# Kernel tuning notes

Hardware: AMD Instinct MI355X
Metric: run time of the kernel (lower is better)

Reference implementation:

```python
import jax, jax.numpy as jnp
import numpy as np

ALPHA = 0.2  # LeakyReLU negative slope
N, F_IN, F_OUT = 8192, 512, 64
NEG_INF = -9e15


def setup_inputs() -> dict:
    key = jax.random.key(0)
    k1, k2, k3, k4 = jax.random.split(key, 4)
    inp = jax.random.normal(k1, (N, F_IN), dtype=jnp.float32)
    adj = jax.random.randint(k2, (N, N), 0, 2, dtype=jnp.int32)
    W = jax.random.normal(k3, (F_IN, F_OUT), dtype=jnp.float32) * (1.414 / np.sqrt(F_IN))
    a = jax.random.normal(k4, (2 * F_OUT, 1), dtype=jnp.float32) * 0.1
    return {"input": inp, "adj": adj, "W": W, "a": a, "sparse": 0}


def reference(input, adj, W, a, sparse):
    h = input @ W  # [N, F_out]
    # Decompose concat([h_i, h_j]) @ a into additive src/dst terms (same math,
    # avoids the O(N^2 * 2F) intermediate): e_ij = leakyrelu(h_i@a1 + h_j@a2)
    f_src = h @ a[:F_OUT]   # [N, 1]
    f_dst = h @ a[F_OUT:]   # [N, 1]
    e = jax.nn.leaky_relu(f_src + f_dst.T, ALPHA)  # [N, N]
    attention = jnp.where(adj > 0, e, NEG_INF)
    attention = jax.nn.softmax(attention, axis=1)
    h_prime = attention @ h  # [N, F_out]
    return jax.nn.leaky_relu(h_prime, 0.01)[None]  # concat=True path; default F.leaky_relu slope 0.01
```

## Files before the change

### kernel.cpp

```cpp
#include <hip/hip_runtime.h>
#include <hip/hip_bf16.h>

#define N 8192
#define FIN 512
#define FOUT 64
#define ALPHA 0.2f

typedef __bf16 bf16x8 __attribute__((ext_vector_type(8)));
typedef float f32x4 __attribute__((ext_vector_type(4)));
typedef int i32x4 __attribute__((ext_vector_type(4)));


__device__ __forceinline__ unsigned enc_f(float x) {
    unsigned u = __float_as_uint(x);
    return (u & 0x80000000u) ? ~u : (u | 0x80000000u);
}
__device__ __forceinline__ float dec_f(unsigned u) {
    return (u & 0x80000000u) ? __uint_as_float(u & 0x7FFFFFFFu) : __uint_as_float(~u);
}

__global__ __launch_bounds__(64) void k_wt(const float* __restrict__ W,
                                           __bf16* __restrict__ WtG) {
    const int g = blockIdx.x * 64 + threadIdx.x;
    const int k = g >> 3;
    const int f0 = (g & 7) * 8;
    const float4 w0 = *(const float4*)(W + (size_t)k * FOUT + f0);
    const float4 w1 = *(const float4*)(W + (size_t)k * FOUT + f0 + 4);
    WtG[(size_t)(f0 + 0) * FIN + k] = (__bf16)w0.x;
    WtG[(size_t)(f0 + 1) * FIN + k] = (__bf16)w0.y;
    WtG[(size_t)(f0 + 2) * FIN + k] = (__bf16)w0.z;
    WtG[(size_t)(f0 + 3) * FIN + k] = (__bf16)w0.w;
    WtG[(size_t)(f0 + 4) * FIN + k] = (__bf16)w1.x;
    WtG[(size_t)(f0 + 5) * FIN + k] = (__bf16)w1.y;
    WtG[(size_t)(f0 + 6) * FIN + k] = (__bf16)w1.z;
    WtG[(size_t)(f0 + 7) * FIN + k] = (__bf16)w1.w;
}

__global__ __launch_bounds__(64) void k12(const float* __restrict__ in,
                                          const __bf16* __restrict__ WtG,
                                          const float* __restrict__ a,
                                          float* __restrict__ f_src,
                                          float* __restrict__ f_dst,
                                          unsigned* __restrict__ Mkey,
                                          __bf16* __restrict__ hT) {
    __shared__ __bf16 tb[64][16];
    const int lane = threadIdx.x;
    const int m = lane & 15, quad = lane >> 4;
    const int i0 = blockIdx.x * 16;

    f32x4 acc[4];
#pragma unroll
    for (int t = 0; t < 4; ++t) acc[t] = (f32x4){0.f, 0.f, 0.f, 0.f};

    const float* arow = in + (size_t)(i0 + m) * FIN + quad * 8;
    for (int k0 = 0; k0 < FIN; k0 += 32) {
        const float4 x0 = *(const float4*)(arow + k0);
        const float4 x1 = *(const float4*)(arow + k0 + 4);
        bf16x8 af;
        af[0] = (__bf16)x0.x; af[1] = (__bf16)x0.y; af[2] = (__bf16)x0.z; af[3] = (__bf16)x0.w;
        af[4] = (__bf16)x1.x; af[5] = (__bf16)x1.y; af[6] = (__bf16)x1.z; af[7] = (__bf16)x1.w;
#pragma unroll
        for (int t = 0; t < 4; ++t) {
            const bf16x8 bf = *(const bf16x8*)(WtG + (size_t)(t * 16 + m) * FIN + k0 + quad * 8);
            acc[t] = __builtin_amdgcn_mfma_f32_16x16x32_bf16(af, bf, acc[t], 0, 0, 0);
        }
    }
    float s1[4], s2[4];
#pragma unroll
    for (int r = 0; r < 4; ++r) { s1[r] = 0.f; s2[r] = 0.f; }
#pragma unroll
    for (int t = 0; t < 4; ++t) {
        const float a1 = a[t * 16 + m], a2 = a[64 + t * 16 + m];
#pragma unroll
        for (int r = 0; r < 4; ++r) {
            s1[r] += acc[t][r] * a1;
            s2[r] += acc[t][r] * a2;
        }
    }
#pragma unroll
    for (int off = 1; off <= 8; off <<= 1)
#pragma unroll
        for (int r = 0; r < 4; ++r) {
            s1[r] += __shfl_xor(s1[r], off);
            s2[r] += __shfl_xor(s2[r], off);
        }
    float lm = -1e30f;
    if (m == 0) {
#pragma unroll
        for (int r = 0; r < 4; ++r) {
            f_src[i0 + quad * 4 + r] = s1[r];
            f_dst[i0 + quad * 4 + r] = s2[r];
            lm = fmaxf(lm, s2[r]);
        }
    }
    lm = fmaxf(lm, __shfl_xor(lm, 16));
    lm = fmaxf(lm, __shfl_xor(lm, 32));
    if (lane == 0) atomicMax(Mkey, enc_f(lm));

#pragma unroll
    for (int t = 0; t < 4; ++t)
#pragma unroll
        for (int r = 0; r < 4; ++r) tb[t * 16 + m][quad * 4 + r] = (__bf16)acc[t][r];
    __syncthreads();
    {
        const int f = lane;
        const bf16x8 v0 = *(const bf16x8*)&tb[f][0];
        const bf16x8 v1 = *(const bf16x8*)&tb[f][8];
        *(bf16x8*)(hT + (size_t)f * N + i0) = v0;
        *(bf16x8*)(hT + (size_t)f * N + i0 + 8) = v1;
    }
}

constexpr int JT = 256;

__global__ __launch_bounds__(256, 4) void k3_attn(const int* __restrict__ adj,
                                                  const float* __restrict__ f_src,
                                                  const float* __restrict__ fdstG,
                                                  const unsigned* __restrict__ Mkey,
                                                  const __bf16* __restrict__ hT,
                                                  float* __restrict__ num,
                                                  float* __restrict__ lsum) {
    __shared__ __bf16 sh[64][JT + 8];
    __shared__ float sfd[JT];
    const int tid = threadIdx.x;
    const int wv = tid >> 6, lane = tid & 63;
    const int m = lane & 15, quad = lane >> 4;
    const int i0 = blockIdx.x * 64 + wv * 16;
    const int jbase = blockIdx.y * 1024;
    const float LOG2E = 1.44269504088896f;

    const float M = dec_f(*Mkey);
    const float fs = f_src[i0 + m];
    const float t0 = fs + M;
    const float shift = fmaxf(t0, ALPHA * t0);

    f32x4 acc[4];
#pragma unroll
    for (int t = 0; t < 4; ++t) acc[t] = (f32x4){0.f, 0.f, 0.f, 0.f};
    f32x4 accl = (f32x4){0.f, 0.f, 0.f, 0.f};

    bf16x8 bones;
#pragma unroll
    for (int jj = 0; jj < 8; ++jj) bones[jj] = (__bf16)(m == 0 ? 1.0f : 0.0f);

    const int* arow = adj + (size_t)(i0 + m) * N;

    for (int jt = jbase; jt < jbase + 1024; jt += JT) {
        __syncthreads();
#pragma unroll
        for (int c = tid; c < 64 * JT / 8; c += 256) {
            const int f = c >> 5, off = (c & 31) * 8;
            *(bf16x8*)&sh[f][off] = *(const bf16x8*)(hT + (size_t)f * N + jt + off);
        }
        if (tid < 64) *(f32x4*)&sfd[tid * 4] = *(const f32x4*)(fdstG + jt + tid * 4);
        __syncthreads();

#pragma unroll
        for (int jj0 = 0; jj0 < JT; jj0 += 64) {
            const int* p = arow + jt + jj0 + quad * 8;
            i32x4 A[4];
            A[0] = __builtin_nontemporal_load((const i32x4*)p);
            A[1] = __builtin_nontemporal_load((const i32x4*)(p + 4));
            A[2] = __builtin_nontemporal_load((const i32x4*)(p + 32));
            A[3] = __builtin_nontemporal_load((const i32x4*)(p + 36));
            const f32x4 D0 = *(const f32x4*)&sfd[jj0 + quad * 8];
            const f32x4 D1 = *(const f32x4*)&sfd[jj0 + quad * 8 + 4];
            const f32x4 D2 = *(const f32x4*)&sfd[jj0 + 32 + quad * 8];
            const f32x4 D3 = *(const f32x4*)&sfd[jj0 + 32 + quad * 8 + 4];
#pragma unroll
            for (int u = 0; u < 2; ++u) {
                const i32x4 Aa = A[u * 2], Ab = A[u * 2 + 1];
                const f32x4 Da = u ? D2 : D0, Db = u ? D3 : D1;
                float wvv[8];
#pragma unroll
                for (int jj = 0; jj < 8; ++jj) {
                    const float fd = jj < 4 ? Da[jj] : Db[jj - 4];
                    const int am = jj < 4 ? Aa[jj] : Ab[jj - 4];
                    float e = fs + fd;
                    e = fmaxf(e, ALPHA * e);
                    const float ex = __builtin_amdgcn_exp2f((e - shift) * LOG2E);
                    wvv[jj] = am > 0 ? ex : 0.f;
                }
                bf16x8 af;
#pragma unroll
                for (int jj = 0; jj < 8; ++jj) af[jj] = (__bf16)wvv[jj];
#pragma unroll
                for (int t = 0; t < 4; ++t) {
                    const bf16x8 bfr =
                        *(const bf16x8*)&sh[t * 16 + m][jj0 + u * 32 + quad * 8];
                    acc[t] = __builtin_amdgcn_mfma_f32_16x16x32_bf16(af, bfr, acc[t], 0, 0, 0);
                }
                accl = __builtin_amdgcn_mfma_f32_16x16x32_bf16(af, bones, accl, 0, 0, 0);
            }
        }
    }
#pragma unroll
    for (int t = 0; t < 4; ++t)
#pragma unroll
        for (int r = 0; r < 4; ++r)
            atomicAdd(&num[(size_t)(i0 + quad * 4 + r) * FOUT + t * 16 + m], acc[t][r]);
    if (m == 0) {
#pragma unroll
        for (int r = 0; r < 4; ++r) atomicAdd(&lsum[i0 + quad * 4 + r], accl[r]);
    }
}

__global__ __launch_bounds__(256) void k4_norm(float* __restrict__ out,
                                               const float* __restrict__ lsum) {
    const int idx = blockIdx.x * 256 + threadIdx.x;
    const float l = lsum[idx >> 6];
    const float v = out[idx] / (l > 0.f ? l : 1.f);
    out[idx] = v > 0.f ? v : 0.01f * v;
}

extern "C" void kernel_launch(void* const* d_in, const int* in_sizes, int n_in,
                              void* d_out, int out_size, void* d_ws, size_t ws_size,
                              hipStream_t stream) {
    const float* in = (const float*)d_in[0];
    const int* adj = (const int*)d_in[1];
    const float* W = (const float*)d_in[2];
    const float* a = (const float*)d_in[3];
    float* out = (float*)d_out;

    char* ws = (char*)d_ws;
    unsigned* Mkey = (unsigned*)ws;
    float* lsum = (float*)(ws + 64);
    float* f_src = (float*)(ws + 32832);
    float* f_dst = (float*)(ws + 65600);
    __bf16* WtG = (__bf16*)(ws + 98368);
    __bf16* hT = (__bf16*)(ws + 163904);

    hipMemsetAsync(ws, 0, 64 + N * 4, stream);
    hipMemsetAsync(d_out, 0, (size_t)N * FOUT * sizeof(float), stream);

    k_wt<<<64, 64, 0, stream>>>(W, WtG);
    k12<<<N / 16, 64, 0, stream>>>(in, WtG, a, f_src, f_dst, Mkey, hT);

    dim3 g3(N / 64, 8);
    k3_attn<<<g3, 256, 0, stream>>>(adj, f_src, f_dst, Mkey, hT, out, lsum);
    k4_norm<<<(N * FOUT) / 256, 256, 0, stream>>>(out, lsum);
}
```

Baseline: 417.7 us.

## Coalesce adj reads across row-contiguous lanes and stage weights through swizzled LDS

The attention kernel now has each wave load 16 adjacency rows with lanes spanning contiguous columns, which gives fully coalesced 1 KB row segments. It computes the exp weights in that layout and writes them to a per-wave XOR-swizzled LDS buffer, then reads them back in MFMA A-fragment layout. The shared h tile and the per-tile barriers are removed, so h fragments are read straight from global memory or cache, and f_dst is loaded once per block. This trades an LDS round trip for the weights and more global traffic for h in exchange for better adj coalescing and fewer syncs.

```diff
diff --git a/kernel.cpp b/kernel.cpp
--- a/kernel.cpp
+++ b/kernel.cpp
@@ -7,6 +7,7 @@
 #define ALPHA 0.2f
 
 typedef __bf16 bf16x8 __attribute__((ext_vector_type(8)));
+typedef __bf16 bf16x4 __attribute__((ext_vector_type(4)));
 typedef float f32x4 __attribute__((ext_vector_type(4)));
 typedef int i32x4 __attribute__((ext_vector_type(4)));
 
@@ -111,8 +112,6 @@
     }
 }
 
-constexpr int JT = 256;
-
 __global__ __launch_bounds__(256, 4) void k3_attn(const int* __restrict__ adj,
                                                   const float* __restrict__ f_src,
                                                   const float* __restrict__ fdstG,
@@ -120,19 +119,27 @@
                                                   const __bf16* __restrict__ hT,
                                                   float* __restrict__ num,
                                                   float* __restrict__ lsum) {
-    __shared__ __bf16 sh[64][JT + 8];
-    __shared__ float sfd[JT];
+    __shared__ float sfd[1024];
+    __shared__ __bf16 wl[4][16][256];
     const int tid = threadIdx.x;
     const int wv = tid >> 6, lane = tid & 63;
     const int m = lane & 15, quad = lane >> 4;
-    const int i0 = blockIdx.x * 64 + wv * 16;
-    const int jbase = blockIdx.y * 1024;
+    const int i0 = __builtin_amdgcn_readfirstlane(blockIdx.x * 64 + wv * 16);
+    const int jb = blockIdx.y * 1024;
     const float LOG2E = 1.44269504088896f;
 
+    *(f32x4*)&sfd[tid * 4] = *(const f32x4*)(fdstG + jb + tid * 4);
+    __syncthreads();
+
     const float M = dec_f(*Mkey);
-    const float fs = f_src[i0 + m];
-    const float t0 = fs + M;
-    const float shift = fmaxf(t0, ALPHA * t0);
+    float fsr[16], shl[16];
+#pragma unroll
+    for (int r = 0; r < 16; ++r) {
+        const float fs = f_src[i0 + r];
+        const float t0 = fs + M;
+        fsr[r] = fs;
+        shl[r] = fmaxf(t0, ALPHA * t0) * LOG2E;
+    }
 
     f32x4 acc[4];
 #pragma unroll
@@ -143,51 +150,39 @@
 #pragma unroll
     for (int jj = 0; jj < 8; ++jj) bones[jj] = (__bf16)(m == 0 ? 1.0f : 0.0f);
 
-    const int* arow = adj + (size_t)(i0 + m) * N;
-
-    for (int jt = jbase; jt < jbase + 1024; jt += JT) {
-        __syncthreads();
-#pragma unroll
-        for (int c = tid; c < 64 * JT / 8; c += 256) {
-            const int f = c >> 5, off = (c & 31) * 8;
-            *(bf16x8*)&sh[f][off] = *(const bf16x8*)(hT + (size_t)f * N + jt + off);
-        }
-        if (tid < 64) *(f32x4*)&sfd[tid * 4] = *(const f32x4*)(fdstG + jt + tid * 4);
-        __syncthreads();
-
-#pragma unroll
-        for (int jj0 = 0; jj0 < JT; jj0 += 64) {
-            const int* p = arow + jt + jj0 + quad * 8;
-            i32x4 A[4];
-            A[0] = __builtin_nontemporal_load((const i32x4*)p);
-            A[1] = __builtin_nontemporal_load((const i32x4*)(p + 4));
-            A[2] = __builtin_nontemporal_load((const i32x4*)(p + 32));
-            A[3] = __builtin_nontemporal_load((const i32x4*)(p + 36));
-            const f32x4 D0 = *(const f32x4*)&sfd[jj0 + quad * 8];
-            const f32x4 D1 = *(const f32x4*)&sfd[jj0 + quad * 8 + 4];
-            const f32x4 D2 = *(const f32x4*)&sfd[jj0 + 32 + quad * 8];
-            const f32x4 D3 = *(const f32x4*)&sfd[jj0 + 32 + quad * 8 + 4];
+    const int* ap = adj + (size_t)i0 * N + jb + lane * 4;
+
+    for (int jt = 0; jt < 1024; jt += 256) {
+        i32x4 adjv[16];
+#pragma unroll
+        for (int r = 0; r < 16; ++r)
+            adjv[r] = __builtin_nontemporal_load((const i32x4*)(ap + (size_t)r * N + jt));
+
+        const f32x4 fd = *(const f32x4*)&sfd[jt + lane * 4];
+
+#pragma unroll
+        for (int r = 0; r < 16; ++r) {
+            bf16x4 wb;
+#pragma unroll
+            for (int c = 0; c < 4; ++c) {
+                float e = fsr[r] + fd[c];
+                e = fmaxf(e, ALPHA * e);
+                const float ex = __builtin_amdgcn_exp2f(e * LOG2E - shl[r]);
+                wb[c] = (__bf16)(adjv[r][c] > 0 ? ex : 0.f);
+            }
+            *(bf16x4*)&wl[wv][r][(lane * 4) ^ ((r & 7) << 3)] = wb;
+        }
+
+#pragma unroll
+        for (int jj0 = 0; jj0 < 256; jj0 += 64) {
 #pragma unroll
             for (int u = 0; u < 2; ++u) {
-                const i32x4 Aa = A[u * 2], Ab = A[u * 2 + 1];
-                const f32x4 Da = u ? D2 : D0, Db = u ? D3 : D1;
-                float wvv[8];
-#pragma unroll
-                for (int jj = 0; jj < 8; ++jj) {
-                    const float fd = jj < 4 ? Da[jj] : Db[jj - 4];
-                    const int am = jj < 4 ? Aa[jj] : Ab[jj - 4];
-                    float e = fs + fd;
-                    e = fmaxf(e, ALPHA * e);
-                    const float ex = __builtin_amdgcn_exp2f((e - shift) * LOG2E);
-                    wvv[jj] = am > 0 ? ex : 0.f;
-                }
-                bf16x8 af;
-#pragma unroll
-                for (int jj = 0; jj < 8; ++jj) af[jj] = (__bf16)wvv[jj];
+                const int cb = jj0 + u * 32 + quad * 8;
+                const bf16x8 af = *(const bf16x8*)&wl[wv][m][cb ^ ((m & 7) << 3)];
 #pragma unroll
                 for (int t = 0; t < 4; ++t) {
                     const bf16x8 bfr =
-                        *(const bf16x8*)&sh[t * 16 + m][jj0 + u * 32 + quad * 8];
+                        *(const bf16x8*)(hT + (size_t)(t * 16 + m) * N + jb + jt + cb);
                     acc[t] = __builtin_amdgcn_mfma_f32_16x16x32_bf16(af, bfr, acc[t], 0, 0, 0);
                 }
                 accl = __builtin_amdgcn_mfma_f32_16x16x32_bf16(af, bones, accl, 0, 0, 0);
```

Result: slower. 449.9 us (+7.7%).
